# Kernel tuning notes

Hardware: AMD Instinct MI355X
Metric: run time of the kernel (lower is better)

## Reference

```python
import jax, jax.numpy as jnp
import numpy as np
from jax import lax

B_, C_IN, IMG, P = 32, 3, 224, 16
D, DEPTH, NCLS = 384, 24, 1000
DI, DS, DCONV, DTR = 2 * D, 16, 4, 24  # d_inner, d_state, d_conv, dt_rank
L = (IMG // P) ** 2 + 1  # 197 tokens incl. cls


def setup_inputs() -> dict:
    key = jax.random.key(0)
    ks = jax.random.split(key, 20)
    s = 0.02
    inp = {
        "x": jax.random.normal(ks[0], (B_, C_IN, IMG, IMG), jnp.float32),
        "patch_w": jax.random.normal(ks[1], (D, C_IN, P, P), jnp.float32) * s,
        "patch_b": jnp.zeros((D,), jnp.float32),
        "cls_token": jax.random.normal(ks[2], (1, 1, D), jnp.float32) * s,
        "pos_embed": jax.random.normal(ks[3], (1, L, D), jnp.float32) * s,
        "ln_w": jnp.ones((DEPTH, D), jnp.float32),
        "ln_b": jnp.zeros((DEPTH, D), jnp.float32),
        "in_proj_w": jax.random.normal(ks[4], (DEPTH, 2 * DI, D), jnp.float32) * s,
        "conv1d_w": jax.random.normal(ks[5], (DEPTH, DI, DCONV), jnp.float32) * s,
        "conv1d_b": jnp.zeros((DEPTH, DI), jnp.float32),
        "x_proj_w": jax.random.normal(ks[6], (DEPTH, DTR + 2 * DS, DI), jnp.float32) * s,
        "dt_proj_w": jax.random.normal(ks[7], (DEPTH, DI, DTR), jnp.float32) * 0.1,
        "dt_proj_b": jax.random.uniform(ks[8], (DEPTH, DI), jnp.float32, -4.0, -2.0),
        "A_log": jnp.tile(jnp.log(jnp.arange(1, DS + 1, dtype=jnp.float32))[None, None, :], (DEPTH, DI, 1)),
        "D_param": jnp.ones((DEPTH, DI), jnp.float32),
        "out_proj_w": jax.random.normal(ks[9], (DEPTH, D, DI), jnp.float32) * s,
        "normf_w": jnp.ones((D,), jnp.float32),
        "normf_b": jnp.zeros((D,), jnp.float32),
        "head_w": jax.random.normal(ks[10], (NCLS, D), jnp.float32) * s,
        "head_b": jnp.zeros((NCLS,), jnp.float32),
    }
    return inp


def _layernorm(x, w, b, eps=1e-5):
    mu = jnp.mean(x, -1, keepdims=True)
    var = jnp.mean(jnp.square(x - mu), -1, keepdims=True)
    return (x - mu) * lax.rsqrt(var + eps) * w + b


def _silu(x):
    return x * jax.nn.sigmoid(x)


def _selective_scan(dA, dBx, Cm):
    # dA, dBx: [B, L, DI, DS]; Cm: [B, L, DS] -> y: [B, L, DI]
    def step(h, inp):
        a, bx, c = inp
        h = a * h + bx
        return h, jnp.einsum("bds,bs->bd", h, c)

    h0 = jnp.zeros((dA.shape[0], DI, DS), dA.dtype)
    _, ys = lax.scan(step, h0, (dA.swapaxes(0, 1), dBx.swapaxes(0, 1), Cm.swapaxes(0, 1)))
    return ys.swapaxes(0, 1)


def _mamba_block(h, p):
    (ln_w, ln_b, in_w, cw, cb, xp_w, dtw, dtb, A_log, Dp, ow) = p
    x = _layernorm(h, ln_w, ln_b)               # [B,L,D]
    xz = jnp.einsum("bld,ed->ble", x, in_w)      # [B,L,2*DI]
    xb, z = jnp.split(xz, 2, axis=-1)
    # causal depthwise conv1d, kernel DCONV
    xc = xb.swapaxes(1, 2)                       # [B,DI,L]
    xc = lax.conv_general_dilated(xc, cw[:, None, :], (1,), [(DCONV - 1, 0)],
                                  feature_group_count=DI,
                                  dimension_numbers=("NCH", "OIH", "NCH"))
    xb = _silu(xc.swapaxes(1, 2) + cb)           # [B,L,DI]
    xdbl = jnp.einsum("bld,ed->ble", xb, xp_w)   # [B,L,DTR+2*DS]
    dt, Bm, Cm = jnp.split(xdbl, [DTR, DTR + DS], axis=-1)
    dt = jax.nn.softplus(jnp.einsum("blr,dr->bld", dt, dtw) + dtb)  # [B,L,DI]
    A = -jnp.exp(A_log)                          # [DI,DS]
    dA = jnp.exp(dt[..., None] * A)              # [B,L,DI,DS]
    dBx = dt[..., None] * Bm[:, :, None, :] * xb[..., None]
    y = _selective_scan(dA, dBx, Cm) + Dp * xb
    y = y * _silu(z)
    out = jnp.einsum("ble,de->bld", y, ow)       # [B,L,D]
    return h + out, None


def reference(x, patch_w, patch_b, cls_token, pos_embed, ln_w, ln_b, in_proj_w,
              conv1d_w, conv1d_b, x_proj_w, dt_proj_w, dt_proj_b, A_log, D_param,
              out_proj_w, normf_w, normf_b, head_w, head_b):
    B = x.shape[0]
    feat = lax.conv_general_dilated(x, patch_w, (P, P), "VALID",
                                    dimension_numbers=("NCHW", "OIHW", "NCHW"))
    feat = feat.reshape(B, D, -1).swapaxes(1, 2) + patch_b  # [B,196,D]
    tok = jnp.concatenate([jnp.broadcast_to(cls_token, (B, 1, D)), feat], axis=1)
    tok = tok + pos_embed
    layer_params = (ln_w, ln_b, in_proj_w, conv1d_w, conv1d_b, x_proj_w,
                    dt_proj_w, dt_proj_b, A_log, D_param, out_proj_w)
    tok, _ = lax.scan(_mamba_block, tok, layer_params)
    tok = _layernorm(tok, normf_w, normf_b)
    return tok[:, 0] @ head_w.T + head_b  # [B, NCLS]
```

## Files before the change

kernel.cpp:

```cpp
#include <hip/hip_runtime.h>
#include <math.h>

#define B_    32
#define D_    384
#define DEPTH 24
#define DI    768
#define DS    16
#define DCONV 4
#define DTR   24
#define L_    197
#define LPAD  208
#define NCLS  1000
#define NTOK  (B_*L_)
#define MPAD  6400
#define NCOMB 896

typedef __bf16 bf16;
typedef __bf16 bf16x2 __attribute__((ext_vector_type(2)));
typedef __bf16 bf16x4 __attribute__((ext_vector_type(4)));
typedef __bf16 bf16x8 __attribute__((ext_vector_type(8)));
typedef float  floatx4 __attribute__((ext_vector_type(4)));

#define INW_E  (1536*384)
#define OUTW_E (384*768)
#define PW_E   (384*768)
#define HW_E   (1024*384)

__device__ __forceinline__ float sigmoidf_(float x){ return 1.f/(1.f+__expf(-x)); }

template<int CTRL>
__device__ __forceinline__ float dppf_(float x){
    return __int_as_float(__builtin_amdgcn_update_dpp(0, __float_as_int(x), CTRL, 0xF, 0xF, true));
}
template<int M>
__device__ __forceinline__ float sxor_(float x){
    if constexpr (M==1)      return dppf_<0xB1>(x);
    else if constexpr (M==2) return dppf_<0x4E>(x);
    else if constexpr (M==4) return dppf_<0x1B>(dppf_<0x141>(x));
    else                     return dppf_<0x128>(x);
}
template<int M>
__device__ __forceinline__ void rlevel_(float* v, const int s){
    const bool hi = (s & M) != 0;
    #pragma unroll
    for (int i = 0; i < M; ++i) {
        const float keep = hi ? v[i+M] : v[i];
        const float send = hi ? v[i] : v[i+M];
        v[i] = keep + sxor_<M>(send);
    }
}

#define INW_ALL  ((long)DEPTH*INW_E)
#define OUTW_ALL ((long)DEPTH*OUTW_E)
#define WCONV_TOT (INW_ALL + OUTW_ALL + PW_E + HW_E)
__global__ void wconv_all_kernel(const float* __restrict__ in_w, const float* __restrict__ out_w,
                                 const float* __restrict__ patch_w, const float* __restrict__ head_w,
                                 bf16* __restrict__ w_in_b, bf16* __restrict__ w_out_b,
                                 bf16* __restrict__ pw_b, bf16* __restrict__ hw_b)
{
    long idx = ((long)blockIdx.x*256 + threadIdx.x)*8;
    if (idx >= WCONV_TOT) return;
    const float* src; bf16* dst; long off;
    bool pad = false;
    if (idx < INW_ALL)                { src = in_w;  dst = w_in_b;  off = idx; }
    else if (idx < INW_ALL+OUTW_ALL)  { src = out_w; dst = w_out_b; off = idx - INW_ALL; }
    else if (idx < INW_ALL+OUTW_ALL+PW_E) { src = patch_w; dst = pw_b; off = idx - INW_ALL - OUTW_ALL; }
    else { off = idx - INW_ALL - OUTW_ALL - PW_E; src = head_w; dst = hw_b; pad = (off >= (long)NCLS*384); }
    bf16x8 r;
    if (pad) {
        #pragma unroll
        for (int j = 0; j < 8; ++j) r[j] = (bf16)0.f;
    } else {
        const float4 a = *(const float4*)(src + off);
        const float4 c = *(const float4*)(src + off + 4);
        r[0]=(bf16)a.x; r[1]=(bf16)a.y; r[2]=(bf16)a.z; r[3]=(bf16)a.w;
        r[4]=(bf16)c.x; r[5]=(bf16)c.y; r[6]=(bf16)c.z; r[7]=(bf16)c.w;
    }
    *(bf16x8*)(dst + off) = r;
}

__global__ void ln_wcomb_kernel(const float* __restrict__ x, const float* __restrict__ w,
                                const float* __restrict__ b, bf16* __restrict__ out,
                                const float* __restrict__ dtw, const float* __restrict__ xpw,
                                bf16* __restrict__ wc)
{
    if (blockIdx.x < NTOK/4) {
        const int row = blockIdx.x*4 + threadIdx.y;
        const int lane = threadIdx.x;
        const float* xr = x + (long)row*D_;
        float v[6]; float s = 0.f;
        #pragma unroll
        for (int i = 0; i < 6; ++i) { v[i] = xr[lane + 64*i]; s += v[i]; }
        #pragma unroll
        for (int o = 32; o; o >>= 1) s += __shfl_xor(s, o, 64);
        const float mu = s * (1.f/384.f);
        float var = 0.f;
        #pragma unroll
        for (int i = 0; i < 6; ++i) { float d = v[i]-mu; var += d*d; }
        #pragma unroll
        for (int o = 32; o; o >>= 1) var += __shfl_xor(var, o, 64);
        const float rstd = rsqrtf(var*(1.f/384.f) + 1e-5f);
        bf16* orow = out + (long)row*D_;
        #pragma unroll
        for (int i = 0; i < 6; ++i) { int c = lane + 64*i; orow[c] = (bf16)((v[i]-mu)*rstd*w[c] + b[c]); }
    } else {
        const int o = blockIdx.x - NTOK/4;
        const int tid = threadIdx.y*64 + threadIdx.x;
        if (o < 768) {
            __shared__ float sw[24];
            if (tid < 24) sw[tid] = dtw[(long)o*DTR + tid];
            __syncthreads();
            for (int i = tid; i < DI; i += 256) {
                float acc = 0.f;
                #pragma unroll
                for (int r = 0; r < 24; ++r) acc += sw[r]*xpw[r*DI + i];
                wc[(long)o*DI + i] = (bf16)acc;
            }
        } else if (o < 800) {
            const float* src = xpw + (long)(o - 768 + 24)*DI;
            for (int i = tid; i < DI; i += 256) wc[(long)o*DI + i] = (bf16)src[i];
        } else {
            for (int i = tid; i < DI; i += 256) wc[(long)o*DI + i] = (bf16)0.f;
        }
    }
}

__global__ void im2col_kernel(const float* __restrict__ x, bf16* __restrict__ patches)
{
    const long idx = (long)blockIdx.x*256 + threadIdx.x;
    if (idx >= (long)B_*196*768) return;
    const int k = idx % 768;
    const int prow = idx / 768;
    const int b = prow / 196, pi = prow % 196;
    const int ph = pi / 14, pw = pi % 14;
    const int c = k >> 8, rem = k & 255, ii = rem >> 4, jj = rem & 15;
    patches[((long)(b*L_ + 1 + pi))*768 + k] =
        (bf16)x[(((long)b*3 + c)*224 + ph*16 + ii)*224 + pw*16 + jj];
}

__global__ void add_pos_kernel(float* __restrict__ tok, const float* __restrict__ pb,
                               const float* __restrict__ pos, const float* __restrict__ cls)
{
    const int idx = blockIdx.x*256 + threadIdx.x;
    if (idx >= NTOK*D_) return;
    const int dd = idx % D_;
    const int row = idx / D_;
    const int p = row % L_;
    if (p == 0) tok[idx] = cls[dd] + pos[dd];
    else        tok[idx] += pb[dd] + pos[p*D_ + dd];
}

template<typename OUT_T>
__global__ void ln_kernel(const float* __restrict__ x, const float* __restrict__ w,
                          const float* __restrict__ b, OUT_T* __restrict__ out,
                          int rows, int xstride, int ostride)
{
    const int row = blockIdx.x*blockDim.y + threadIdx.y;
    if (row >= rows) return;
    const int lane = threadIdx.x;
    const float* xr = x + (long)row*xstride;
    float v[6]; float s = 0.f;
    #pragma unroll
    for (int i = 0; i < 6; ++i) { v[i] = xr[lane + 64*i]; s += v[i]; }
    #pragma unroll
    for (int o = 32; o; o >>= 1) s += __shfl_xor(s, o, 64);
    const float mu = s * (1.f/384.f);
    float var = 0.f;
    #pragma unroll
    for (int i = 0; i < 6; ++i) { float d = v[i]-mu; var += d*d; }
    #pragma unroll
    for (int o = 32; o; o >>= 1) var += __shfl_xor(var, o, 64);
    const float rstd = rsqrtf(var*(1.f/384.f) + 1e-5f);
    OUT_T* orow = out + (long)row*ostride;
    #pragma unroll
    for (int i = 0; i < 6; ++i) { int c = lane + 64*i; orow[c] = (OUT_T)((v[i]-mu)*rstd*w[c] + b[c]); }
}

template<int BM, int ACC, typename CT>
__global__ __launch_bounds__(256)
void gemm_bf16_kernel(const bf16* __restrict__ A, const bf16* __restrict__ B,
                      CT* __restrict__ C, int M, int N, int K)
{
    constexpr int ASLABS = BM/16;
    constexpr int NJ = (BM == 128) ? 4 : 2;
    __shared__ bf16 As[BM*32];
    __shared__ bf16 Bs[128*32];
    const int tid  = threadIdx.x;
    const int wave = tid >> 6, lane = tid & 63;
    const int bm = blockIdx.x*BM, bn = blockIdx.y*128;
    const int wm = (BM == 128) ? (wave>>1)*64 : 0;
    const int wn = (BM == 128) ? (wave&1)*64 : wave*32;
    floatx4 acc[4][NJ];
    #pragma unroll
    for (int i=0;i<4;++i)
        #pragma unroll
        for (int j=0;j<NJ;++j) acc[i][j] = (floatx4){0.f,0.f,0.f,0.f};

    const int lrow = lane >> 2;
    const int lcol = (lane & 3) * 8;
    const int am = lane & 15, ak = (lane>>4)*8;

    for (int k0 = 0; k0 < K; k0 += 32) {
        #pragma unroll
        for (int s = wave; s < ASLABS + 8; s += 4) {
            if (s < ASLABS) {
                const bf16* ga = A + (long)(bm + s*16 + lrow)*K + k0 + lcol;
                __builtin_amdgcn_global_load_lds(
                    (const __attribute__((address_space(1))) void*)ga,
                    (__attribute__((address_space(3))) void*)(As + s*512), 16, 0, 0);
            } else {
                const int s2 = s - ASLABS;
                const bf16* gb = B + (long)(bn + s2*16 + lrow)*K + k0 + lcol;
                __builtin_amdgcn_global_load_lds(
                    (const __attribute__((address_space(1))) void*)gb,
                    (__attribute__((address_space(3))) void*)(Bs + s2*512), 16, 0, 0);
            }
        }
        __syncthreads();
        bf16x8 af[4], bff[NJ];
        #pragma unroll
        for (int i=0;i<4;++i) af[i]  = *(const bf16x8*)(As + (wm + i*16 + am)*32 + ak);
        #pragma unroll
        for (int j=0;j<NJ;++j) bff[j] = *(const bf16x8*)(Bs + (wn + j*16 + am)*32 + ak);
        #pragma unroll
        for (int i=0;i<4;++i)
            #pragma unroll
            for (int j=0;j<NJ;++j)
                acc[i][j] = __builtin_amdgcn_mfma_f32_16x16x32_bf16(af[i], bff[j], acc[i][j], 0, 0, 0);
        __syncthreads();
    }
    const int rbase = bm + wm + (lane>>4)*4;
    const int cbase = bn + wn + (lane & 15);
    #pragma unroll
    for (int i = 0; i < 4; ++i) {
        #pragma unroll
        for (int r = 0; r < 4; ++r) {
            const int row = rbase + i*16 + r;
            if (row >= M) continue;
            #pragma unroll
            for (int j = 0; j < NJ; ++j) {
                const long idx = (long)row*N + cbase + j*16;
                if (ACC) C[idx] += acc[i][j][r];
                else     C[idx]  = (CT)acc[i][j][r];
            }
        }
    }
}

__global__ void conv_silu_kernel(const bf16* __restrict__ xz, const float* __restrict__ cw,
                                 const float* __restrict__ cb, bf16* __restrict__ out)
{
    const int idx = blockIdx.x*256 + threadIdx.x;
    if (idx >= NTOK*96) return;
    const int g  = idx % 96;
    const int bl = idx / 96;
    const int l  = bl % L_;
    const int di = g*8;
    const long rowbase = (long)(bl - l)*(2*DI) + di;
    bf16x8 xv[4];
    #pragma unroll
    for (int k = 0; k < 4; ++k) {
        const int lt = l - 3 + k;
        if (lt >= 0) {
            xv[k] = *(const bf16x8*)(xz + rowbase + (long)lt*(2*DI));
        } else {
            #pragma unroll
            for (int j = 0; j < 8; ++j) xv[k][j] = (bf16)0.f;
        }
    }
    bf16x8 r;
    #pragma unroll
    for (int j = 0; j < 8; ++j) {
        const float4 wj = ((const float4*)cw)[di + j];
        float a = cb[di + j];
        a += wj.x*(float)xv[0][j] + wj.y*(float)xv[1][j] + wj.z*(float)xv[2][j] + wj.w*(float)xv[3][j];
        r[j] = (bf16)(a * sigmoidf_(a));
    }
    *(bf16x8*)(out + (long)bl*DI + di) = r;
}

__global__ __launch_bounds__(256)
void scan_kernel(const bf16* __restrict__ xbc, const bf16* __restrict__ comb,
                 const bf16* __restrict__ xz, const float* __restrict__ A_log,
                 const float* __restrict__ Dp, const float* __restrict__ dtb,
                 bf16* __restrict__ y)
{
    const int tid  = threadIdx.x;
    const int w    = tid >> 6, lane = tid & 63;
    const int s    = lane & 15;
    const int dlq  = lane >> 4;
    const int dl   = w*4 + dlq;
    const int bx   = blockIdx.x;
    const int cblk = (bx & 7)*6 + (bx >> 3);
    const int di0  = cblk*16;
    const int di   = di0 + dl;
    const int b    = blockIdx.y;

    const float A2_s = -__expf(A_log[di*DS + s]) * 1.44269504f;
    const float Dv   = Dp[di];

    __shared__ __align__(16) bf16x2 sh_dt2[(LPAD/2)*32];
    __shared__ __align__(16) bf16x2 sh_bc2[(LPAD/2)*32];

    const long base = (long)b*L_;
    const int e = tid & 15;
    const float bias = dtb[di0 + e];
    for (int idx = tid; idx < LPAD*16; idx += 256) {
        const int t = idx >> 4;
        const int idx2 = (t >> 1)*32 + 2*e + (t & 1);
        bf16x2 dtdx; dtdx[0] = (bf16)0.f; dtdx[1] = (bf16)0.f;
        bf16x2 bc;   bc[0] = (bf16)0.f;   bc[1] = (bf16)0.f;
        if (t < L_) {
            const long row = base + t;
            const float xv = (float)xbc[row*DI + di0 + e];
            const float dr = (float)comb[row*NCOMB + di0 + e] + bias;
            const float dtv = (dr > 20.f) ? dr : __logf(1.f + __expf(dr));
            dtdx[0] = (bf16)dtv; dtdx[1] = (bf16)(dtv*xv);
            bc[0] = comb[row*NCOMB + 768 + e];
            bc[1] = comb[row*NCOMB + 784 + e];
        }
        sh_dt2[idx2] = dtdx;
        sh_bc2[idx2] = bc;
    }
    __syncthreads();

    const bf16x4* dt4 = (const bf16x4*)sh_dt2;
    const bf16x4* bc4 = (const bf16x4*)sh_bc2;

    float h = 0.f;
    for (int c = 0; c < LPAD/16; ++c) {
        float v[16];
        #pragma unroll
        for (int t2 = 0; t2 < 8; ++t2) {
            const int g2 = c*8 + t2;
            const bf16x4 q  = dt4[g2*16 + dl];
            const bf16x4 bc = bc4[g2*16 + s];
            const float a0 = __builtin_amdgcn_exp2f((float)q[0] * A2_s);
            h = fmaf(a0, h, (float)q[1] * (float)bc[0]);
            v[2*t2]   = h * (float)bc[1];
            const float a1 = __builtin_amdgcn_exp2f((float)q[2] * A2_s);
            h = fmaf(a1, h, (float)q[3] * (float)bc[2]);
            v[2*t2+1] = h * (float)bc[3];
        }
        const int gt = c*16 + s;
        const long row = base + gt;
        float xv = 0.f, zv = 0.f;
        if (gt < L_) {
            xv = (float)xbc[row*DI + di];
            zv = (float)xz[row*(2*DI) + DI + di];
        }
        rlevel_<8>(v, s); rlevel_<4>(v, s); rlevel_<2>(v, s); rlevel_<1>(v, s);
        if (gt < L_) {
            y[row*DI + di] = (bf16)((v[0] + Dv*xv) * zv * sigmoidf_(zv));
        }
    }
}

__global__ void head_bias_kernel(const float* __restrict__ chead, const float* __restrict__ hb,
                                 float* __restrict__ out)
{
    const int idx = blockIdx.x*256 + threadIdx.x;
    if (idx >= B_*NCLS) return;
    const int n = idx % NCLS, b = idx / NCLS;
    out[idx] = chead[(long)b*1024 + n] + hb[n];
}

extern "C" void kernel_launch(void* const* d_in, const int* in_sizes, int n_in,
                              void* d_out, int out_size, void* d_ws, size_t ws_size,
                              hipStream_t stream)
{
    const float* x       = (const float*)d_in[0];
    const float* patch_w = (const float*)d_in[1];
    const float* patch_b = (const float*)d_in[2];
    const float* cls_tok = (const float*)d_in[3];
    const float* pos_emb = (const float*)d_in[4];
    const float* ln_w    = (const float*)d_in[5];
    const float* ln_b    = (const float*)d_in[6];
    const float* in_w    = (const float*)d_in[7];
    const float* conv_w  = (const float*)d_in[8];
    const float* conv_b  = (const float*)d_in[9];
    const float* xp_w    = (const float*)d_in[10];
    const float* dt_w    = (const float*)d_in[11];
    const float* dt_b    = (const float*)d_in[12];
    const float* A_log   = (const float*)d_in[13];
    const float* D_par   = (const float*)d_in[14];
    const float* out_w   = (const float*)d_in[15];
    const float* normf_w = (const float*)d_in[16];
    const float* normf_b = (const float*)d_in[17];
    const float* head_w  = (const float*)d_in[18];
    const float* head_b  = (const float*)d_in[19];
    float* out = (float*)d_out;

    char* p = (char*)d_ws;
    float* tok    = (float*)p;  p += (long)NTOK*D_*4;
    bf16*  xz_b   = (bf16*)p;   p += (long)MPAD*2*DI*2;
    bf16*  xbc_b  = (bf16*)p;   p += (long)MPAD*DI*2;
    bf16*  y_b    = (bf16*)p;   p += (long)MPAD*DI*2;
    bf16*  comb_b = (bf16*)p;   p += (long)MPAD*NCOMB*2;
    bf16*  xnorm_b= (bf16*)p;   p += (long)MPAD*D_*2;
    bf16*  ln0_b  = (bf16*)p;   p += (long)64*D_*2;
    float* chead  = (float*)p;  p += (long)64*1024*4;
    bf16*  wcomb_b= (bf16*)p;   p += (long)NCOMB*DI*2;
    bf16*  w_in_b = (bf16*)p;   p += (long)DEPTH*INW_E*2;
    bf16*  w_out_b= (bf16*)p;   p += (long)DEPTH*OUTW_E*2;
    bf16*  pw_b   = (bf16*)p;   p += (long)PW_E*2;
    bf16*  hw_b   = (bf16*)p;   p += (long)HW_E*2;
    bf16*  patches = comb_b;

    wconv_all_kernel<<<dim3((WCONV_TOT/8 + 255)/256), 256, 0, stream>>>(
        in_w, out_w, patch_w, head_w, w_in_b, w_out_b, pw_b, hw_b);

    im2col_kernel<<<dim3(((long)B_*196*768 + 255)/256), 256, 0, stream>>>(x, patches);
    gemm_bf16_kernel<64,0,float><<<dim3(100, 3), 256, 0, stream>>>(
        patches, pw_b, tok, NTOK, D_, 768);
    add_pos_kernel<<<dim3((NTOK*D_ + 255)/256), 256, 0, stream>>>(tok, patch_b, pos_emb, cls_tok);

    for (int layer = 0; layer < DEPTH; ++layer) {
        ln_wcomb_kernel<<<dim3(NTOK/4 + NCOMB), dim3(64,4), 0, stream>>>(
            tok, ln_w + layer*D_, ln_b + layer*D_, xnorm_b,
            dt_w + (long)layer*DI*DTR, xp_w + (long)layer*56*768, wcomb_b);
        gemm_bf16_kernel<128,0,bf16><<<dim3(50, 12), 256, 0, stream>>>(
            xnorm_b, w_in_b + (long)layer*INW_E, xz_b, NTOK, 2*DI, D_);
        conv_silu_kernel<<<dim3((NTOK*96 + 255)/256), 256, 0, stream>>>(
            xz_b, conv_w + layer*DI*DCONV, conv_b + layer*DI, xbc_b);
        gemm_bf16_kernel<128,0,bf16><<<dim3(50, 7), 256, 0, stream>>>(
            xbc_b, wcomb_b, comb_b, NTOK, NCOMB, DI);
        scan_kernel<<<dim3(48, B_), 256, 0, stream>>>(
            xbc_b, comb_b, xz_b, A_log + layer*DI*DS, D_par + layer*DI,
            dt_b + layer*DI, y_b);
        gemm_bf16_kernel<64,1,float><<<dim3(100, 3), 256, 0, stream>>>(
            y_b, w_out_b + (long)layer*OUTW_E, tok, NTOK, D_, DI);
    }

    ln_kernel<bf16><<<dim3(8), dim3(64,4), 0, stream>>>(tok, normf_w, normf_b, ln0_b, B_, L_*D_, D_);
    gemm_bf16_kernel<64,0,float><<<dim3(1, 8), 256, 0, stream>>>(
        ln0_b, hw_b, chead, 64, 1024, D_);
    head_bias_kernel<<<dim3((B_*NCLS + 255)/256), 256, 0, stream>>>(chead, head_b, out);
}
```

Measured before the change: 3.159 ms.

## Unfuse dt projection into two low-rank GEMMs instead of combined weight

Replaces the per-layer precomputed combined weight (dt_proj·x_proj, 896x768) with two GEMMs: x_proj (768→128 padded) and then dt_proj over the 32-padded rank. The x_proj and dt_proj weights are converted to bf16 once in the bulk weight conversion kernel, and the layernorm kernel no longer builds the combined weight each layer. This cuts the main GEMM FLOPs and removes the per-layer weight-combination work, at the cost of an extra kernel launch and an intermediate buffer round trip. The GEMM gains an lda parameter so the second GEMM can read the first 32 columns of the 128-wide intermediate.

Result: faster. 3.027 ms (-4.2%).

```diff
diff --git a/kernel.cpp b/kernel.cpp
--- a/kernel.cpp
+++ b/kernel.cpp
@@ -13,7 +13,8 @@
 #define NCLS  1000
 #define NTOK  (B_*L_)
 #define MPAD  6400
-#define NCOMB 896
+#define NXP   128
+#define KDT   32
 
 typedef __bf16 bf16;
 typedef __bf16 bf16x2 __attribute__((ext_vector_type(2)));
@@ -25,6 +26,8 @@
 #define OUTW_E (384*768)
 #define PW_E   (384*768)
 #define HW_E   (1024*384)
+#define XPW_E  (NXP*768)
+#define DTW_E  (768*KDT)
 
 __device__ __forceinline__ float sigmoidf_(float x){ return 1.f/(1.f+__expf(-x)); }
 
@@ -52,20 +55,42 @@
 
 #define INW_ALL  ((long)DEPTH*INW_E)
 #define OUTW_ALL ((long)DEPTH*OUTW_E)
-#define WCONV_TOT (INW_ALL + OUTW_ALL + PW_E + HW_E)
+#define XPW_ALL  ((long)DEPTH*XPW_E)
+#define DTW_ALL  ((long)DEPTH*DTW_E)
+#define SEG1 (INW_ALL)
+#define SEG2 (SEG1 + OUTW_ALL)
+#define SEG3 (SEG2 + PW_E)
+#define SEG4 (SEG3 + HW_E)
+#define SEG5 (SEG4 + XPW_ALL)
+#define WCONV_TOT (SEG5 + DTW_ALL)
 __global__ void wconv_all_kernel(const float* __restrict__ in_w, const float* __restrict__ out_w,
                                  const float* __restrict__ patch_w, const float* __restrict__ head_w,
+                                 const float* __restrict__ xp_w, const float* __restrict__ dt_w,
                                  bf16* __restrict__ w_in_b, bf16* __restrict__ w_out_b,
-                                 bf16* __restrict__ pw_b, bf16* __restrict__ hw_b)
+                                 bf16* __restrict__ pw_b, bf16* __restrict__ hw_b,
+                                 bf16* __restrict__ xpw_b, bf16* __restrict__ dtw_b)
 {
     long idx = ((long)blockIdx.x*256 + threadIdx.x)*8;
     if (idx >= WCONV_TOT) return;
     const float* src; bf16* dst; long off;
     bool pad = false;
-    if (idx < INW_ALL)                { src = in_w;  dst = w_in_b;  off = idx; }
-    else if (idx < INW_ALL+OUTW_ALL)  { src = out_w; dst = w_out_b; off = idx - INW_ALL; }
-    else if (idx < INW_ALL+OUTW_ALL+PW_E) { src = patch_w; dst = pw_b; off = idx - INW_ALL - OUTW_ALL; }
-    else { off = idx - INW_ALL - OUTW_ALL - PW_E; src = head_w; dst = hw_b; pad = (off >= (long)NCLS*384); }
+    if (idx < SEG1)       { src = in_w;  dst = w_in_b;  off = idx; }
+    else if (idx < SEG2)  { src = out_w; dst = w_out_b; off = idx - SEG1; }
+    else if (idx < SEG3)  { src = patch_w; dst = pw_b; off = idx - SEG2; }
+    else if (idx < SEG4)  { off = idx - SEG3; src = head_w; dst = hw_b; pad = (off >= (long)NCLS*384); }
+    else if (idx < SEG5)  {
+        off = idx - SEG4; dst = xpw_b;
+        const int layer = off / XPW_E; const int rem = off % XPW_E;
+        const int r = rem / 768, c = rem % 768;
+        pad = (r >= 56);
+        src = xp_w + ((long)layer*56 + r)*768 + c - off;
+    } else {
+        off = idx - SEG5; dst = dtw_b;
+        const int layer = off / DTW_E; const int rem = off % DTW_E;
+        const int di = rem / KDT, c = rem % KDT;
+        pad = (c >= 24);
+        src = dt_w + ((long)layer*768 + di)*24 + c - off;
+    }
     bf16x8 r;
     if (pad) {
         #pragma unroll
@@ -77,52 +102,6 @@
         r[4]=(bf16)c.x; r[5]=(bf16)c.y; r[6]=(bf16)c.z; r[7]=(bf16)c.w;
     }
     *(bf16x8*)(dst + off) = r;
-}
-
-__global__ void ln_wcomb_kernel(const float* __restrict__ x, const float* __restrict__ w,
-                                const float* __restrict__ b, bf16* __restrict__ out,
-                                const float* __restrict__ dtw, const float* __restrict__ xpw,
-                                bf16* __restrict__ wc)
-{
-    if (blockIdx.x < NTOK/4) {
-        const int row = blockIdx.x*4 + threadIdx.y;
-        const int lane = threadIdx.x;
-        const float* xr = x + (long)row*D_;
-        float v[6]; float s = 0.f;
-        #pragma unroll
-        for (int i = 0; i < 6; ++i) { v[i] = xr[lane + 64*i]; s += v[i]; }
-        #pragma unroll
-        for (int o = 32; o; o >>= 1) s += __shfl_xor(s, o, 64);
-        const float mu = s * (1.f/384.f);
-        float var = 0.f;
-        #pragma unroll
-        for (int i = 0; i < 6; ++i) { float d = v[i]-mu; var += d*d; }
-        #pragma unroll
-        for (int o = 32; o; o >>= 1) var += __shfl_xor(var, o, 64);
-        const float rstd = rsqrtf(var*(1.f/384.f) + 1e-5f);
-        bf16* orow = out + (long)row*D_;
-        #pragma unroll
-        for (int i = 0; i < 6; ++i) { int c = lane + 64*i; orow[c] = (bf16)((v[i]-mu)*rstd*w[c] + b[c]); }
-    } else {
-        const int o = blockIdx.x - NTOK/4;
-        const int tid = threadIdx.y*64 + threadIdx.x;
-        if (o < 768) {
-            __shared__ float sw[24];
-            if (tid < 24) sw[tid] = dtw[(long)o*DTR + tid];
-            __syncthreads();
-            for (int i = tid; i < DI; i += 256) {
-                float acc = 0.f;
-                #pragma unroll
-                for (int r = 0; r < 24; ++r) acc += sw[r]*xpw[r*DI + i];
-                wc[(long)o*DI + i] = (bf16)acc;
-            }
-        } else if (o < 800) {
-            const float* src = xpw + (long)(o - 768 + 24)*DI;
-            for (int i = tid; i < DI; i += 256) wc[(long)o*DI + i] = (bf16)src[i];
-        } else {
-            for (int i = tid; i < DI; i += 256) wc[(long)o*DI + i] = (bf16)0.f;
-        }
-    }
 }
 
 __global__ void im2col_kernel(const float* __restrict__ x, bf16* __restrict__ patches)
@@ -179,7 +158,7 @@
 template<int BM, int ACC, typename CT>
 __global__ __launch_bounds__(256)
 void gemm_bf16_kernel(const bf16* __restrict__ A, const bf16* __restrict__ B,
-                      CT* __restrict__ C, int M, int N, int K)
+                      CT* __restrict__ C, int M, int N, int K, int lda)
 {
     constexpr int ASLABS = BM/16;
     constexpr int NJ = (BM == 128) ? 4 : 2;
@@ -204,7 +183,7 @@
         #pragma unroll
         for (int s = wave; s < ASLABS + 8; s += 4) {
             if (s < ASLABS) {
-                const bf16* ga = A + (long)(bm + s*16 + lrow)*K + k0 + lcol;
+                const bf16* ga = A + (long)(bm + s*16 + lrow)*lda + k0 + lcol;
                 __builtin_amdgcn_global_load_lds(
                     (const __attribute__((address_space(1))) void*)ga,
                     (__attribute__((address_space(3))) void*)(As + s*512), 16, 0, 0);
@@ -280,10 +259,10 @@
 }
 
 __global__ __launch_bounds__(256)
-void scan_kernel(const bf16* __restrict__ xbc, const bf16* __restrict__ comb,
-                 const bf16* __restrict__ xz, const float* __restrict__ A_log,
-                 const float* __restrict__ Dp, const float* __restrict__ dtb,
-                 bf16* __restrict__ y)
+void scan_kernel(const bf16* __restrict__ xbc, const bf16* __restrict__ dtc,
+                 const bf16* __restrict__ tmp, const bf16* __restrict__ xz,
+                 const float* __restrict__ A_log, const float* __restrict__ Dp,
+                 const float* __restrict__ dtb, bf16* __restrict__ y)
 {
     const int tid  = threadIdx.x;
     const int w    = tid >> 6, lane = tid & 63;
@@ -313,11 +292,11 @@
         if (t < L_) {
             const long row = base + t;
             const float xv = (float)xbc[row*DI + di0 + e];
-            const float dr = (float)comb[row*NCOMB + di0 + e] + bias;
+            const float dr = (float)dtc[row*DI + di0 + e] + bias;
             const float dtv = (dr > 20.f) ? dr : __logf(1.f + __expf(dr));
             dtdx[0] = (bf16)dtv; dtdx[1] = (bf16)(dtv*xv);
-            bc[0] = comb[row*NCOMB + 768 + e];
-            bc[1] = comb[row*NCOMB + 784 + e];
+            bc[0] = tmp[row*NXP + 24 + e];
+            bc[1] = tmp[row*NXP + 40 + e];
         }
         sh_dt2[idx2] = dtdx;
         sh_bc2[idx2] = bc;
@@ -396,44 +375,48 @@
     bf16*  xz_b   = (bf16*)p;   p += (long)MPAD*2*DI*2;
     bf16*  xbc_b  = (bf16*)p;   p += (long)MPAD*DI*2;
     bf16*  y_b    = (bf16*)p;   p += (long)MPAD*DI*2;
-    bf16*  comb_b = (bf16*)p;   p += (long)MPAD*NCOMB*2;
-    bf16*  xnorm_b= (bf16*)p;   p += (long)MPAD*D_*2;
+    bf16*  dtc_b  = (bf16*)p;   p += (long)MPAD*DI*2;
+    bf16*  tmp_b  = (bf16*)p;   p += (long)MPAD*NXP*2;
     bf16*  ln0_b  = (bf16*)p;   p += (long)64*D_*2;
     float* chead  = (float*)p;  p += (long)64*1024*4;
-    bf16*  wcomb_b= (bf16*)p;   p += (long)NCOMB*DI*2;
     bf16*  w_in_b = (bf16*)p;   p += (long)DEPTH*INW_E*2;
     bf16*  w_out_b= (bf16*)p;   p += (long)DEPTH*OUTW_E*2;
     bf16*  pw_b   = (bf16*)p;   p += (long)PW_E*2;
     bf16*  hw_b   = (bf16*)p;   p += (long)HW_E*2;
-    bf16*  patches = comb_b;
+    bf16*  xpw_b  = (bf16*)p;   p += (long)DEPTH*XPW_E*2;
+    bf16*  dtw_b  = (bf16*)p;   p += (long)DEPTH*DTW_E*2;
+    bf16*  patches = dtc_b;
+    bf16*  xnorm_b = y_b;
 
     wconv_all_kernel<<<dim3((WCONV_TOT/8 + 255)/256), 256, 0, stream>>>(
-        in_w, out_w, patch_w, head_w, w_in_b, w_out_b, pw_b, hw_b);
+        in_w, out_w, patch_w, head_w, xp_w, dt_w,
+        w_in_b, w_out_b, pw_b, hw_b, xpw_b, dtw_b);
 
     im2col_kernel<<<dim3(((long)B_*196*768 + 255)/256), 256, 0, stream>>>(x, patches);
     gemm_bf16_kernel<64,0,float><<<dim3(100, 3), 256, 0, stream>>>(
-        patches, pw_b, tok, NTOK, D_, 768);
+        patches, pw_b, tok, NTOK, D_, 768, 768);
     add_pos_kernel<<<dim3((NTOK*D_ + 255)/256), 256, 0, stream>>>(tok, patch_b, pos_emb, cls_tok);
 
     for (int layer = 0; layer < DEPTH; ++layer) {
-        ln_wcomb_kernel<<<dim3(NTOK/4 + NCOMB), dim3(64,4), 0, stream>>>(
-            tok, ln_w + layer*D_, ln_b + layer*D_, xnorm_b,
-            dt_w + (long)layer*DI*DTR, xp_w + (long)layer*56*768, wcomb_b);
+        ln_kernel<bf16><<<dim3(NTOK/4), dim3(64,4), 0, stream>>>(
+            tok, ln_w + layer*D_, ln_b + layer*D_, xnorm_b, NTOK, D_, D_);
         gemm_bf16_kernel<128,0,bf16><<<dim3(50, 12), 256, 0, stream>>>(
-            xnorm_b, w_in_b + (long)layer*INW_E, xz_b, NTOK, 2*DI, D_);
+            xnorm_b, w_in_b + (long)layer*INW_E, xz_b, NTOK, 2*DI, D_, D_);
         conv_silu_kernel<<<dim3((NTOK*96 + 255)/256), 256, 0, stream>>>(
             xz_b, conv_w + layer*DI*DCONV, conv_b + layer*DI, xbc_b);
-        gemm_bf16_kernel<128,0,bf16><<<dim3(50, 7), 256, 0, stream>>>(
-            xbc_b, wcomb_b, comb_b, NTOK, NCOMB, DI);
+        gemm_bf16_kernel<64,0,bf16><<<dim3(100, 1), 256, 0, stream>>>(
+            xbc_b, xpw_b + (long)layer*XPW_E, tmp_b, NTOK, NXP, DI, DI);
+        gemm_bf16_kernel<64,0,bf16><<<dim3(100, 6), 256, 0, stream>>>(
+            tmp_b, dtw_b + (long)layer*DTW_E, dtc_b, NTOK, DI, KDT, NXP);
         scan_kernel<<<dim3(48, B_), 256, 0, stream>>>(
-            xbc_b, comb_b, xz_b, A_log + layer*DI*DS, D_par + layer*DI,
+            xbc_b, dtc_b, tmp_b, xz_b, A_log + layer*DI*DS, D_par + layer*DI,
             dt_b + layer*DI, y_b);
         gemm_bf16_kernel<64,1,float><<<dim3(100, 3), 256, 0, stream>>>(
-            y_b, w_out_b + (long)layer*OUTW_E, tok, NTOK, D_, DI);
+            y_b, w_out_b + (long)layer*OUTW_E, tok, NTOK, D_, DI, DI);
     }
 
     ln_kernel<bf16><<<dim3(8), dim3(64,4), 0, stream>>>(tok, normf_w, normf_b, ln0_b, B_, L_*D_, D_);
     gemm_bf16_kernel<64,0,float><<<dim3(1, 8), 256, 0, stream>>>(
-        ln0_b, hw_b, chead, 64, 1024, D_);
+        ln0_b, hw_b, chead, 64, 1024, D_, D_);
     head_bias_kernel<<<dim3((B_*NCLS + 255)/256), 256, 0, stream>>>(chead, head_b, out);
 }
```
